# Kernel tuning notes

Measured on AMD Instinct MI355X. Metric: run time of the kernel, lower is better.

Reference implementation:

```python
import jax, jax.numpy as jnp
import numpy as np

ALPHA = 0.2  # LeakyReLU negative slope


def setup_inputs() -> dict:
    key = jax.random.key(0)
    k1, k2, k3, k4 = jax.random.split(key, 4)
    N, IN, OUT = 8192, 512, 256
    x = jax.random.normal(k1, (N, IN), dtype=jnp.float32)
    adj = jnp.zeros((N, N), dtype=jnp.float32)  # accepted but unused by the module
    W = jax.random.normal(k2, (OUT, IN), dtype=jnp.float32) * (1.0 / np.sqrt(IN))
    a1 = jax.random.normal(k3, (OUT,), dtype=jnp.float32) * (1.0 / np.sqrt(OUT))
    a2 = jax.random.normal(k4, (OUT,), dtype=jnp.float32) * (1.0 / np.sqrt(OUT))
    return {"x": x, "adj": adj, "W": W, "a1": a1, "a2": a2}


def reference(x, adj, W, a1, a2):
    # h = tran(x): [N, OUT]
    h = x @ W.T
    # additive GAT scores: e[i, j] = a2 . h_i + a1 . h_j  (from unsqueeze(0)+unsqueeze(1))
    s1 = h @ a1  # [N], att1(h)
    s2 = h @ a2  # [N], att2(h)
    e = s2[:, None] + s1[None, :]  # [N, N]
    e = jnp.where(e > 0, e, ALPHA * e)  # LeakyReLU
    attn = jax.nn.softmax(e, axis=1)  # softmax over dim=1; dropout is identity in eval
    return attn @ h  # [N, OUT]
```

## Files before the change

kernel.cpp:

```cpp
#include <hip/hip_runtime.h>

#define NROW 8192
#define DIN  512
#define DOUT 256
#define NCHUNK 256
#define CLEN 32

constexpr size_t OFF_H      = 0;
constexpr size_t OFF_S1     = OFF_H + (size_t)NROW*DOUT*4;
constexpr size_t OFF_S2     = OFF_S1 + NROW*4;
constexpr size_t OFF_RANK   = OFF_S2 + NROW*4;
constexpr size_t OFF_MISC   = OFF_RANK + NROW*4;
constexpr size_t MEMSET_LEN = OFF_MISC + 256 - OFF_S1;
constexpr size_t OFF_S1S    = OFF_MISC + 256;
constexpr size_t OFF_PERM   = OFF_S1S + NROW*4;
constexpr size_t OFF_WHI    = OFF_PERM + NROW*4;
constexpr size_t OFF_WLO    = OFF_WHI + NROW*4;
constexpr size_t OFF_PRELOS = OFF_WLO + NROW*4;
constexpr size_t OFF_SUFHIS = OFF_PRELOS + 33024;
constexpr size_t OFF_CSLO   = OFF_SUFHIS + 33024;
constexpr size_t OFF_CSHI   = OFF_CSLO + 1024;
constexpr size_t OFF_TLO    = OFF_CSHI + 1024;
constexpr size_t OFF_THI    = OFF_TLO + (size_t)NCHUNK*DOUT*4;
constexpr size_t OFF_PRELO  = OFF_THI + (size_t)NCHUNK*DOUT*4;
constexpr size_t OFF_SUFHI  = OFF_PRELO + (size_t)(NROW+1)*DOUT*4;
constexpr size_t OFF_XHI    = OFF_SUFHI + (size_t)(NROW+1)*DOUT*4;
constexpr size_t OFF_XLO    = OFF_XHI + (size_t)NROW*DIN*2;
constexpr size_t OFF_BHI    = OFF_XLO + (size_t)NROW*DIN*2;
constexpr size_t OFF_BLO    = OFF_BHI + (size_t)DOUT*DIN*2;
constexpr size_t WS_NEED    = OFF_BLO + (size_t)DOUT*DIN*2;

typedef float f32x4 __attribute__((ext_vector_type(4)));
typedef short s16x8 __attribute__((ext_vector_type(8)));

__device__ __forceinline__ unsigned short bf16_rne(float f) {
  unsigned int u = __float_as_uint(f);
  return (unsigned short)((u + 0x7fffu + ((u >> 16) & 1u)) >> 16);
}

__global__ __launch_bounds__(256) void split_inputs(const float* __restrict__ x,
                                                    const float* __restrict__ W,
                                                    unsigned short* __restrict__ Xhi,
                                                    unsigned short* __restrict__ Xlo,
                                                    unsigned short* __restrict__ Bhi,
                                                    unsigned short* __restrict__ Blo) {
  const int b = blockIdx.x;
  const float* src;
  unsigned short *dh, *dl;
  size_t off;
  if (b < 2048) {
    off = ((size_t)b * 256 + threadIdx.x) * 8;
    src = x; dh = Xhi; dl = Xlo;
  } else {
    off = ((size_t)(b - 2048) * 256 + threadIdx.x) * 8;
    src = W; dh = Bhi; dl = Blo;
  }
  float4 u = *(const float4*)(src + off);
  float4 v = *(const float4*)(src + off + 4);
  float f[8] = {u.x, u.y, u.z, u.w, v.x, v.y, v.z, v.w};
  s16x8 hv, lv;
#pragma unroll
  for (int j = 0; j < 8; ++j) {
    unsigned short hh = bf16_rne(f[j]);
    float r = f[j] - __uint_as_float(((unsigned int)hh) << 16);
    hv[j] = (short)hh;
    lv[j] = (short)bf16_rne(r);
  }
  *(s16x8*)(dh + off) = hv;
  *(s16x8*)(dl + off) = lv;
}

__global__ __launch_bounds__(256) void gemm_h_mfma(const unsigned short* __restrict__ Xhi,
                                                   const unsigned short* __restrict__ Xlo,
                                                   const unsigned short* __restrict__ Bhi,
                                                   const unsigned short* __restrict__ Blo,
                                                   const float* __restrict__ a1,
                                                   const float* __restrict__ a2,
                                                   float* __restrict__ h,
                                                   float* __restrict__ s1,
                                                   float* __restrict__ s2) {
  __shared__ unsigned short AsH[64][40], AsL[64][40], BsH[64][40], BsL[64][40];
  const int tid = threadIdx.x;
  const int bid = blockIdx.x;
  const int swz = (bid & 7) * 64 + (bid >> 3);
  const int rowBase = (swz >> 2) * 64;
  const int colBase = (swz & 3) * 64;
  const int wid = tid >> 6, lane = tid & 63;
  const int wRow = wid >> 1, wCol = wid & 1;
  const int lhi = lane >> 4, llo = lane & 15;

  f32x4 acc[2][2];
#pragma unroll
  for (int m = 0; m < 2; ++m)
#pragma unroll
    for (int n = 0; n < 2; ++n) acc[m][n] = (f32x4)(0.f);

  const int sr = tid >> 2;
  const int sq = tid & 3;
  const unsigned short* xh = Xhi + (size_t)(rowBase + sr) * DIN + sq * 8;
  const unsigned short* xl = Xlo + (size_t)(rowBase + sr) * DIN + sq * 8;
  const unsigned short* bh = Bhi + (size_t)(colBase + sr) * DIN + sq * 8;
  const unsigned short* bl = Blo + (size_t)(colBase + sr) * DIN + sq * 8;

  s16x8 rah = *(const s16x8*)(xh);
  s16x8 ral = *(const s16x8*)(xl);
  s16x8 rbh = *(const s16x8*)(bh);
  s16x8 rbl = *(const s16x8*)(bl);

  for (int k0 = 0; k0 < DIN; k0 += 32) {
    __syncthreads();
    *(s16x8*)&AsH[sr][sq * 8] = rah;
    *(s16x8*)&AsL[sr][sq * 8] = ral;
    *(s16x8*)&BsH[sr][sq * 8] = rbh;
    *(s16x8*)&BsL[sr][sq * 8] = rbl;
    __syncthreads();
    if (k0 + 32 < DIN) {
      rah = *(const s16x8*)(xh + k0 + 32);
      ral = *(const s16x8*)(xl + k0 + 32);
      rbh = *(const s16x8*)(bh + k0 + 32);
      rbl = *(const s16x8*)(bl + k0 + 32);
    }
    s16x8 afh[2], afl[2], bfh[2], bfl[2];
#pragma unroll
    for (int m = 0; m < 2; ++m) {
      afh[m] = *(const s16x8*)&AsH[wRow * 32 + m * 16 + llo][lhi * 8];
      afl[m] = *(const s16x8*)&AsL[wRow * 32 + m * 16 + llo][lhi * 8];
    }
#pragma unroll
    for (int n = 0; n < 2; ++n) {
      bfh[n] = *(const s16x8*)&BsH[wCol * 32 + n * 16 + llo][lhi * 8];
      bfl[n] = *(const s16x8*)&BsL[wCol * 32 + n * 16 + llo][lhi * 8];
    }
#pragma unroll
    for (int m = 0; m < 2; ++m)
#pragma unroll
      for (int n = 0; n < 2; ++n) {
        acc[m][n] = __builtin_amdgcn_mfma_f32_16x16x32_bf16(afh[m], bfh[n], acc[m][n], 0, 0, 0);
        acc[m][n] = __builtin_amdgcn_mfma_f32_16x16x32_bf16(afl[m], bfh[n], acc[m][n], 0, 0, 0);
        acc[m][n] = __builtin_amdgcn_mfma_f32_16x16x32_bf16(afh[m], bfl[n], acc[m][n], 0, 0, 0);
      }
  }
  float a1c[2], a2c[2];
#pragma unroll
  for (int n = 0; n < 2; ++n) {
    const int col = colBase + wCol * 32 + n * 16 + llo;
    a1c[n] = a1[col];
    a2c[n] = a2[col];
  }
#pragma unroll
  for (int m = 0; m < 2; ++m) {
    float p1[4] = {0.f, 0.f, 0.f, 0.f}, p2[4] = {0.f, 0.f, 0.f, 0.f};
#pragma unroll
    for (int n = 0; n < 2; ++n) {
      const int col = colBase + wCol * 32 + n * 16 + llo;
#pragma unroll
      for (int j = 0; j < 4; ++j) {
        const int row = rowBase + wRow * 32 + m * 16 + lhi * 4 + j;
        h[(size_t)row * DOUT + col] = acc[m][n][j];
        p1[j] = fmaf(acc[m][n][j], a1c[n], p1[j]);
        p2[j] = fmaf(acc[m][n][j], a2c[n], p2[j]);
      }
    }
#pragma unroll
    for (int j = 0; j < 4; ++j) {
#pragma unroll
      for (int msk = 1; msk < 16; msk <<= 1) {
        p1[j] += __shfl_xor(p1[j], msk);
        p2[j] += __shfl_xor(p2[j], msk);
      }
    }
    if (llo == 0) {
#pragma unroll
      for (int j = 0; j < 4; ++j) {
        const int row = rowBase + wRow * 32 + m * 16 + lhi * 4 + j;
        atomicAdd(&s1[row], p1[j]);
        atomicAdd(&s2[row], p2[j]);
      }
    }
  }
}

__global__ __launch_bounds__(256) void rank_count(const float* __restrict__ s1,
                                                  int* __restrict__ rank,
                                                  unsigned int* __restrict__ miscu) {
  __shared__ float sj[1024];
  __shared__ float wm[4];
  const int t = threadIdx.x;
  const int ib = blockIdx.x, jc = blockIdx.y;
  const int j0 = jc * 1024;
  *(float4*)&sj[t << 2] = *(const float4*)(s1 + j0 + (t << 2));
  const int i = ib * 256 + t;
  const float v = s1[i];
  __syncthreads();
  int cnt = 0;
#pragma unroll 4
  for (int q = 0; q < 256; ++q) {
    float4 sv = *(const float4*)&sj[q << 2];
    int jg = j0 + (q << 2);
    cnt += (int)(sv.x < v) + (int)((sv.x == v) & (jg + 0 < i));
    cnt += (int)(sv.y < v) + (int)((sv.y == v) & (jg + 1 < i));
    cnt += (int)(sv.z < v) + (int)((sv.z == v) & (jg + 2 < i));
    cnt += (int)(sv.w < v) + (int)((sv.w == v) & (jg + 3 < i));
  }
  atomicAdd(&rank[i], cnt);
  if (jc == 0) {
    float m = v;
#pragma unroll
    for (int off = 32; off > 0; off >>= 1) m = fmaxf(m, __shfl_down(m, off));
    if ((t & 63) == 0) wm[t >> 6] = m;
    __syncthreads();
    if (t == 0) {
      float mm = fmaxf(fmaxf(wm[0], wm[1]), fmaxf(wm[2], wm[3]));
      unsigned int b = __float_as_uint(mm);
      unsigned int enc = (b & 0x80000000u) ? ~b : (b | 0x80000000u);
      atomicMax(miscu, enc);
    }
  }
}

__global__ __launch_bounds__(256) void scatter_w(const float* __restrict__ s1,
                                                 const int* __restrict__ rank,
                                                 const unsigned int* __restrict__ miscu,
                                                 float* __restrict__ miscf,
                                                 float* __restrict__ s1s,
                                                 int* __restrict__ perm,
                                                 float* __restrict__ w_hi,
                                                 float* __restrict__ w_lo) {
  const int i = blockIdx.x * 256 + threadIdx.x;
  unsigned int e = miscu[0];
  unsigned int b = (e & 0x80000000u) ? (e & 0x7fffffffu) : ~e;
  const float M1 = __uint_as_float(b);
  const float v = s1[i];
  const int r = rank[i];
  s1s[r] = v;
  perm[r] = i;
  w_hi[r] = __expf(v - M1);
  w_lo[r] = __expf(0.2f * (v - M1));
  if (i == 0) miscf[0] = M1;
}

__global__ __launch_bounds__(256) void chunk_totals(const float* __restrict__ h,
                                                    const int* __restrict__ perm,
                                                    const float* __restrict__ w_hi,
                                                    const float* __restrict__ w_lo,
                                                    float* __restrict__ T_lo,
                                                    float* __restrict__ T_hi,
                                                    float* __restrict__ cs_lo,
                                                    float* __restrict__ cs_hi) {
  const int d = threadIdx.x, b = blockIdx.x;
  const int j0 = b * CLEN;
  float tlo = 0.f, thi = 0.f;
#pragma unroll
  for (int e = 0; e < CLEN; e += 4) {
    int4 p4 = *(const int4*)(perm + j0 + e);
    float4 wl4 = *(const float4*)(w_lo + j0 + e);
    float4 wh4 = *(const float4*)(w_hi + j0 + e);
    float h0 = h[(size_t)p4.x * DOUT + d];
    float h1 = h[(size_t)p4.y * DOUT + d];
    float h2 = h[(size_t)p4.z * DOUT + d];
    float h3 = h[(size_t)p4.w * DOUT + d];
    tlo += wl4.x * h0 + wl4.y * h1 + wl4.z * h2 + wl4.w * h3;
    thi += wh4.x * h0 + wh4.y * h1 + wh4.z * h2 + wh4.w * h3;
  }
  T_lo[b * DOUT + d] = tlo;
  T_hi[b * DOUT + d] = thi;
  if (d < 64) {
    float wl = (d < 32) ? w_lo[j0 + d] : 0.f;
    float wh = (d < 32) ? w_hi[j0 + d] : 0.f;
#pragma unroll
    for (int off = 32; off > 0; off >>= 1) {
      wl += __shfl_down(wl, off);
      wh += __shfl_down(wh, off);
    }
    if (d == 0) { cs_lo[b] = wl; cs_hi[b] = wh; }
  }
}

__global__ __launch_bounds__(256) void write_prefix(const float* __restrict__ h,
                                                    const int* __restrict__ perm,
                                                    const float* __restrict__ w_hi,
                                                    const float* __restrict__ w_lo,
                                                    const float* __restrict__ T_lo,
                                                    const float* __restrict__ T_hi,
                                                    const float* __restrict__ cs_lo,
                                                    const float* __restrict__ cs_hi,
                                                    float* __restrict__ PreLo,
                                                    float* __restrict__ SufHi,
                                                    float* __restrict__ prelo_s,
                                                    float* __restrict__ sufhi_s) {
  const int d = threadIdx.x, b = blockIdx.x;
  const int j0 = b * CLEN;
  if (d < 64) {
    float accp = 0.f, acct = 0.f;
    for (int p = d; p < NCHUNK; p += 64) {
      float cl = cs_lo[p], ch = cs_hi[p];
      accp += (p < b) ? cl : 0.f;
      acct += (p > b) ? ch : 0.f;
    }
#pragma unroll
    for (int off = 32; off > 0; off >>= 1) {
      accp += __shfl_down(accp, off);
      acct += __shfl_down(acct, off);
    }
    float pres  = __shfl(accp, 0);
    float tails = __shfl(acct, 0);
    float wl = (d < 32) ? w_lo[j0 + d] : 0.f;
    float wh = (d < 32) ? w_hi[j0 + d] : 0.f;
    float pl = wl, ph = wh;
#pragma unroll
    for (int off = 1; off < 32; off <<= 1) {
      float a = __shfl_up(pl, off);
      float c = __shfl_up(ph, off);
      if (d >= off) { pl += a; ph += c; }
    }
    float chunk_hi_tot = __shfl(ph, 31);
    if (d < 32) {
      prelo_s[j0 + d] = pres + (pl - wl);
      sufhi_s[j0 + d] = tails + (chunk_hi_tot - (ph - wh));
    }
    if (b == NCHUNK - 1 && d == 31) {
      prelo_s[NROW] = pres + pl;
      sufhi_s[NROW] = 0.f;
    }
  }
  float rl = 0.f, tail = 0.f;
#pragma unroll 4
  for (int p = 0; p < b; ++p)           rl   += T_lo[p * DOUT + d];
#pragma unroll 4
  for (int p = b + 1; p < NCHUNK; ++p)  tail += T_hi[p * DOUT + d];
  float phl[CLEN], phh[CLEN];
  float ownHi = 0.f;
#pragma unroll
  for (int e = 0; e < CLEN; e += 4) {
    int4 p4 = *(const int4*)(perm + j0 + e);
    float4 wl4 = *(const float4*)(w_lo + j0 + e);
    float4 wh4 = *(const float4*)(w_hi + j0 + e);
    float h0 = h[(size_t)p4.x * DOUT + d];
    float h1 = h[(size_t)p4.y * DOUT + d];
    float h2 = h[(size_t)p4.z * DOUT + d];
    float h3 = h[(size_t)p4.w * DOUT + d];
    phl[e + 0] = wl4.x * h0; phl[e + 1] = wl4.y * h1;
    phl[e + 2] = wl4.z * h2; phl[e + 3] = wl4.w * h3;
    phh[e + 0] = wh4.x * h0; phh[e + 1] = wh4.y * h1;
    phh[e + 2] = wh4.z * h2; phh[e + 3] = wh4.w * h3;
    ownHi += phh[e + 0] + phh[e + 1] + phh[e + 2] + phh[e + 3];
  }
  float shb = tail + ownHi;
  float preh = 0.f;
#pragma unroll
  for (int e = 0; e < CLEN; ++e) {
    size_t j = (size_t)(j0 + e);
    PreLo[j * DOUT + d] = rl;
    SufHi[j * DOUT + d] = shb - preh;
    rl   += phl[e];
    preh += phh[e];
  }
  if (b == NCHUNK - 1) {
    PreLo[(size_t)NROW * DOUT + d] = rl;
    SufHi[(size_t)NROW * DOUT + d] = 0.f;
  }
}

__global__ __launch_bounds__(256) void finalize(const float* __restrict__ s2,
                                                const float* __restrict__ s1s,
                                                const float* __restrict__ miscf,
                                                const float* __restrict__ PreLo,
                                                const float* __restrict__ SufHi,
                                                const float* __restrict__ prelo_s,
                                                const float* __restrict__ sufhi_s,
                                                float* __restrict__ out) {
  const int wave = threadIdx.x >> 6, lane = threadIdx.x & 63;
  const int i = blockIdx.x * 4 + wave;
  const float c = s2[i];
  const float M1 = miscf[0];
  const float tval = -c;
  int lo = 0, hi = NROW;
  while (lo < hi) {
    int mid = (lo + hi) >> 1;
    if (s1s[mid] <= tval) lo = mid + 1; else hi = mid;
  }
  const int k = lo;
  const float u = c + M1;
  const float m = fmaxf(u, 0.2f * u);
  const float fh = __expf(u - m);
  const float fl = __expf(0.2f * u - m);
  const float den = fh * sufhi_s[k] + fl * prelo_s[k];
  const float inv = 1.f / den;
  float4 A = *(const float4*)(SufHi + (size_t)k * DOUT + (lane << 2));
  float4 B = *(const float4*)(PreLo + (size_t)k * DOUT + (lane << 2));
  float4 o;
  o.x = (fh * A.x + fl * B.x) * inv;
  o.y = (fh * A.y + fl * B.y) * inv;
  o.z = (fh * A.z + fl * B.z) * inv;
  o.w = (fh * A.w + fl * B.w) * inv;
  *(float4*)(out + (size_t)i * DOUT + (lane << 2)) = o;
}

extern "C" void kernel_launch(void* const* d_in, const int* in_sizes, int n_in,
                              void* d_out, int out_size, void* d_ws, size_t ws_size,
                              hipStream_t stream) {
  const float* x  = (const float*)d_in[0];
  const float* W  = (const float*)d_in[2];
  const float* a1 = (const float*)d_in[3];
  const float* a2 = (const float*)d_in[4];
  float* out = (float*)d_out;

  char* ws = (char*)d_ws;
  if (ws_size < WS_NEED) ws = (char*)d_in[1];

  float*          h       = (float*)(ws + OFF_H);
  float*          s1      = (float*)(ws + OFF_S1);
  float*          s2      = (float*)(ws + OFF_S2);
  int*            rank    = (int*)  (ws + OFF_RANK);
  unsigned int*   miscu   = (unsigned int*)(ws + OFF_MISC);
  float*          miscf   = (float*)(ws + OFF_MISC) + 1;
  float*          s1s     = (float*)(ws + OFF_S1S);
  int*            perm    = (int*)  (ws + OFF_PERM);
  float*          w_hi    = (float*)(ws + OFF_WHI);
  float*          w_lo    = (float*)(ws + OFF_WLO);
  float*          prelo_s = (float*)(ws + OFF_PRELOS);
  float*          sufhi_s = (float*)(ws + OFF_SUFHIS);
  float*          cs_lo   = (float*)(ws + OFF_CSLO);
  float*          cs_hi   = (float*)(ws + OFF_CSHI);
  float*          T_lo    = (float*)(ws + OFF_TLO);
  float*          T_hi    = (float*)(ws + OFF_THI);
  float*          PreLo   = (float*)(ws + OFF_PRELO);
  float*          SufHi   = (float*)(ws + OFF_SUFHI);
  unsigned short* Xhi     = (unsigned short*)(ws + OFF_XHI);
  unsigned short* Xlo     = (unsigned short*)(ws + OFF_XLO);
  unsigned short* Bhi     = (unsigned short*)(ws + OFF_BHI);
  unsigned short* Blo     = (unsigned short*)(ws + OFF_BLO);

  hipMemsetAsync(s1, 0, MEMSET_LEN, stream);

  split_inputs<<<2048 + 64, 256, 0, stream>>>(x, W, Xhi, Xlo, Bhi, Blo);
  gemm_h_mfma<<<512, 256, 0, stream>>>(Xhi, Xlo, Bhi, Blo, a1, a2, h, s1, s2);
  rank_count<<<dim3(NROW / 256, 8), 256, 0, stream>>>(s1, rank, miscu);
  scatter_w<<<NROW / 256, 256, 0, stream>>>(s1, rank, miscu, miscf, s1s, perm, w_hi, w_lo);
  chunk_totals<<<NCHUNK, 256, 0, stream>>>(h, perm, w_hi, w_lo, T_lo, T_hi, cs_lo, cs_hi);
  write_prefix<<<NCHUNK, 256, 0, stream>>>(h, perm, w_hi, w_lo, T_lo, T_hi, cs_lo, cs_hi,
                                           PreLo, SufHi, prelo_s, sufhi_s);
  finalize<<<NROW / 4, 256, 0, stream>>>(s2, s1s, miscf, PreLo, SufHi, prelo_s, sufhi_s, out);
}
```

Measured before the change: 387.9 us.

## Fuse bf16 hi/lo split of x and W into the GEMM prologue

Removes the separate split_inputs kernel that wrote bf16 hi/lo copies of x and W to global memory. The GEMM now loads fp32 directly, converts to hi/lo in registers, and stages 64-wide K tiles in shared memory. K-steps per tile double and the next tile's loads are overlapped with MFMA work. This saves a kernel launch and roughly 16 MB of global write-plus-read traffic, at the cost of more registers and LDS per block and conversion ALU work inside the GEMM. W is also converted redundantly by every row block.

```diff
diff --git a/kernel.cpp b/kernel.cpp
--- a/kernel.cpp
+++ b/kernel.cpp
@@ -24,11 +24,7 @@
 constexpr size_t OFF_THI    = OFF_TLO + (size_t)NCHUNK*DOUT*4;
 constexpr size_t OFF_PRELO  = OFF_THI + (size_t)NCHUNK*DOUT*4;
 constexpr size_t OFF_SUFHI  = OFF_PRELO + (size_t)(NROW+1)*DOUT*4;
-constexpr size_t OFF_XHI    = OFF_SUFHI + (size_t)(NROW+1)*DOUT*4;
-constexpr size_t OFF_XLO    = OFF_XHI + (size_t)NROW*DIN*2;
-constexpr size_t OFF_BHI    = OFF_XLO + (size_t)NROW*DIN*2;
-constexpr size_t OFF_BLO    = OFF_BHI + (size_t)DOUT*DIN*2;
-constexpr size_t WS_NEED    = OFF_BLO + (size_t)DOUT*DIN*2;
+constexpr size_t WS_NEED    = OFF_SUFHI + (size_t)(NROW+1)*DOUT*4;
 
 typedef float f32x4 __attribute__((ext_vector_type(4)));
 typedef short s16x8 __attribute__((ext_vector_type(8)));
@@ -38,48 +34,26 @@
   return (unsigned short)((u + 0x7fffu + ((u >> 16) & 1u)) >> 16);
 }
 
-__global__ __launch_bounds__(256) void split_inputs(const float* __restrict__ x,
-                                                    const float* __restrict__ W,
-                                                    unsigned short* __restrict__ Xhi,
-                                                    unsigned short* __restrict__ Xlo,
-                                                    unsigned short* __restrict__ Bhi,
-                                                    unsigned short* __restrict__ Blo) {
-  const int b = blockIdx.x;
-  const float* src;
-  unsigned short *dh, *dl;
-  size_t off;
-  if (b < 2048) {
-    off = ((size_t)b * 256 + threadIdx.x) * 8;
-    src = x; dh = Xhi; dl = Xlo;
-  } else {
-    off = ((size_t)(b - 2048) * 256 + threadIdx.x) * 8;
-    src = W; dh = Bhi; dl = Blo;
-  }
-  float4 u = *(const float4*)(src + off);
-  float4 v = *(const float4*)(src + off + 4);
+__device__ __forceinline__ void cvt8_pair(const float4 u, const float4 v,
+                                          s16x8& hi, s16x8& lo) {
   float f[8] = {u.x, u.y, u.z, u.w, v.x, v.y, v.z, v.w};
-  s16x8 hv, lv;
 #pragma unroll
   for (int j = 0; j < 8; ++j) {
     unsigned short hh = bf16_rne(f[j]);
     float r = f[j] - __uint_as_float(((unsigned int)hh) << 16);
-    hv[j] = (short)hh;
-    lv[j] = (short)bf16_rne(r);
-  }
-  *(s16x8*)(dh + off) = hv;
-  *(s16x8*)(dl + off) = lv;
-}
-
-__global__ __launch_bounds__(256) void gemm_h_mfma(const unsigned short* __restrict__ Xhi,
-                                                   const unsigned short* __restrict__ Xlo,
-                                                   const unsigned short* __restrict__ Bhi,
-                                                   const unsigned short* __restrict__ Blo,
+    hi[j] = (short)hh;
+    lo[j] = (short)bf16_rne(r);
+  }
+}
+
+__global__ __launch_bounds__(256) void gemm_h_mfma(const float* __restrict__ x,
+                                                   const float* __restrict__ W,
                                                    const float* __restrict__ a1,
                                                    const float* __restrict__ a2,
                                                    float* __restrict__ h,
                                                    float* __restrict__ s1,
                                                    float* __restrict__ s2) {
-  __shared__ unsigned short AsH[64][40], AsL[64][40], BsH[64][40], BsL[64][40];
+  __shared__ unsigned short AsH[64][72], AsL[64][72], BsH[64][72], BsL[64][72];
   const int tid = threadIdx.x;
   const int bid = blockIdx.x;
   const int swz = (bid & 7) * 64 + (bid >> 3);
@@ -95,50 +69,70 @@
 #pragma unroll
     for (int n = 0; n < 2; ++n) acc[m][n] = (f32x4)(0.f);
 
-  const int sr = tid >> 2;
-  const int sq = tid & 3;
-  const unsigned short* xh = Xhi + (size_t)(rowBase + sr) * DIN + sq * 8;
-  const unsigned short* xl = Xlo + (size_t)(rowBase + sr) * DIN + sq * 8;
-  const unsigned short* bh = Bhi + (size_t)(colBase + sr) * DIN + sq * 8;
-  const unsigned short* bl = Blo + (size_t)(colBase + sr) * DIN + sq * 8;
-
-  s16x8 rah = *(const s16x8*)(xh);
-  s16x8 ral = *(const s16x8*)(xl);
-  s16x8 rbh = *(const s16x8*)(bh);
-  s16x8 rbl = *(const s16x8*)(bl);
-
-  for (int k0 = 0; k0 < DIN; k0 += 32) {
+  const int tr = tid >> 2;
+  const int tq = tid & 3;
+  const float* px = x + (size_t)(rowBase + tr) * DIN + tq * 16;
+  const float* pw = W + (size_t)(colBase + tr) * DIN + tq * 16;
+
+  s16x8 cAh[2], cAl[2], cBh[2], cBl[2];
+  {
+    float4 a0 = *(const float4*)(px + 0),  a1v = *(const float4*)(px + 4);
+    float4 a2v = *(const float4*)(px + 8), a3 = *(const float4*)(px + 12);
+    float4 b0 = *(const float4*)(pw + 0),  b1 = *(const float4*)(pw + 4);
+    float4 b2 = *(const float4*)(pw + 8),  b3 = *(const float4*)(pw + 12);
+    cvt8_pair(a0, a1v, cAh[0], cAl[0]);
+    cvt8_pair(a2v, a3, cAh[1], cAl[1]);
+    cvt8_pair(b0, b1, cBh[0], cBl[0]);
+    cvt8_pair(b2, b3, cBh[1], cBl[1]);
+  }
+
+  for (int k0 = 0; k0 < DIN; k0 += 64) {
     __syncthreads();
-    *(s16x8*)&AsH[sr][sq * 8] = rah;
-    *(s16x8*)&AsL[sr][sq * 8] = ral;
-    *(s16x8*)&BsH[sr][sq * 8] = rbh;
-    *(s16x8*)&BsL[sr][sq * 8] = rbl;
+    *(s16x8*)&AsH[tr][tq * 16 + 0] = cAh[0];
+    *(s16x8*)&AsH[tr][tq * 16 + 8] = cAh[1];
+    *(s16x8*)&AsL[tr][tq * 16 + 0] = cAl[0];
+    *(s16x8*)&AsL[tr][tq * 16 + 8] = cAl[1];
+    *(s16x8*)&BsH[tr][tq * 16 + 0] = cBh[0];
+    *(s16x8*)&BsH[tr][tq * 16 + 8] = cBh[1];
+    *(s16x8*)&BsL[tr][tq * 16 + 0] = cBl[0];
+    *(s16x8*)&BsL[tr][tq * 16 + 8] = cBl[1];
     __syncthreads();
-    if (k0 + 32 < DIN) {
-      rah = *(const s16x8*)(xh + k0 + 32);
-      ral = *(const s16x8*)(xl + k0 + 32);
-      rbh = *(const s16x8*)(bh + k0 + 32);
-      rbl = *(const s16x8*)(bl + k0 + 32);
-    }
-    s16x8 afh[2], afl[2], bfh[2], bfl[2];
-#pragma unroll
-    for (int m = 0; m < 2; ++m) {
-      afh[m] = *(const s16x8*)&AsH[wRow * 32 + m * 16 + llo][lhi * 8];
-      afl[m] = *(const s16x8*)&AsL[wRow * 32 + m * 16 + llo][lhi * 8];
-    }
-#pragma unroll
-    for (int n = 0; n < 2; ++n) {
-      bfh[n] = *(const s16x8*)&BsH[wCol * 32 + n * 16 + llo][lhi * 8];
-      bfl[n] = *(const s16x8*)&BsL[wCol * 32 + n * 16 + llo][lhi * 8];
-    }
-#pragma unroll
-    for (int m = 0; m < 2; ++m)
+    const bool more = (k0 + 64 < DIN);
+    float4 a0, a1v, a2v, a3, b0, b1, b2, b3;
+    if (more) {
+      a0 = *(const float4*)(px + k0 + 64 + 0);  a1v = *(const float4*)(px + k0 + 64 + 4);
+      a2v = *(const float4*)(px + k0 + 64 + 8); a3 = *(const float4*)(px + k0 + 64 + 12);
+      b0 = *(const float4*)(pw + k0 + 64 + 0);  b1 = *(const float4*)(pw + k0 + 64 + 4);
+      b2 = *(const float4*)(pw + k0 + 64 + 8);  b3 = *(const float4*)(pw + k0 + 64 + 12);
+    }
+#pragma unroll
+    for (int kk = 0; kk < 64; kk += 32) {
+      s16x8 afh[2], afl[2], bfh[2], bfl[2];
+#pragma unroll
+      for (int m = 0; m < 2; ++m) {
+        afh[m] = *(const s16x8*)&AsH[wRow * 32 + m * 16 + llo][kk + lhi * 8];
+        afl[m] = *(const s16x8*)&AsL[wRow * 32 + m * 16 + llo][kk + lhi * 8];
+      }
 #pragma unroll
       for (int n = 0; n < 2; ++n) {
-        acc[m][n] = __builtin_amdgcn_mfma_f32_16x16x32_bf16(afh[m], bfh[n], acc[m][n], 0, 0, 0);
-        acc[m][n] = __builtin_amdgcn_mfma_f32_16x16x32_bf16(afl[m], bfh[n], acc[m][n], 0, 0, 0);
-        acc[m][n] = __builtin_amdgcn_mfma_f32_16x16x32_bf16(afh[m], bfl[n], acc[m][n], 0, 0, 0);
+        bfh[n] = *(const s16x8*)&BsH[wCol * 32 + n * 16 + llo][kk + lhi * 8];
+        bfl[n] = *(const s16x8*)&BsL[wCol * 32 + n * 16 + llo][kk + lhi * 8];
       }
+#pragma unroll
+      for (int m = 0; m < 2; ++m)
+#pragma unroll
+        for (int n = 0; n < 2; ++n) {
+          acc[m][n] = __builtin_amdgcn_mfma_f32_16x16x32_bf16(afh[m], bfh[n], acc[m][n], 0, 0, 0);
+          acc[m][n] = __builtin_amdgcn_mfma_f32_16x16x32_bf16(afl[m], bfh[n], acc[m][n], 0, 0, 0);
+          acc[m][n] = __builtin_amdgcn_mfma_f32_16x16x32_bf16(afh[m], bfl[n], acc[m][n], 0, 0, 0);
+        }
+    }
+    if (more) {
+      cvt8_pair(a0, a1v, cAh[0], cAl[0]);
+      cvt8_pair(a2v, a3, cAh[1], cAl[1]);
+      cvt8_pair(b0, b1, cBh[0], cBl[0]);
+      cvt8_pair(b2, b3, cBh[1], cBl[1]);
+    }
   }
   float a1c[2], a2c[2];
 #pragma unroll
@@ -426,15 +420,10 @@
   float*          T_hi    = (float*)(ws + OFF_THI);
   float*          PreLo   = (float*)(ws + OFF_PRELO);
   float*          SufHi   = (float*)(ws + OFF_SUFHI);
-  unsigned short* Xhi     = (unsigned short*)(ws + OFF_XHI);
-  unsigned short* Xlo     = (unsigned short*)(ws + OFF_XLO);
-  unsigned short* Bhi     = (unsigned short*)(ws + OFF_BHI);
-  unsigned short* Blo     = (unsigned short*)(ws + OFF_BLO);
 
   hipMemsetAsync(s1, 0, MEMSET_LEN, stream);
 
-  split_inputs<<<2048 + 64, 256, 0, stream>>>(x, W, Xhi, Xlo, Bhi, Blo);
-  gemm_h_mfma<<<512, 256, 0, stream>>>(Xhi, Xlo, Bhi, Blo, a1, a2, h, s1, s2);
+  gemm_h_mfma<<<512, 256, 0, stream>>>(x, W, a1, a2, h, s1, s2);
   rank_count<<<dim3(NROW / 256, 8), 256, 0, stream>>>(s1, rank, miscu);
   scatter_w<<<NROW / 256, 256, 0, stream>>>(s1, rank, miscu, miscf, s1s, perm, w_hi, w_lo);
   chunk_totals<<<NCHUNK, 256, 0, stream>>>(h, perm, w_hi, w_lo, T_lo, T_hi, cs_lo, cs_hi);
```

Measured after the change: 384.7 us. No clear change (-0.8%).
